# Kernel tuning notes

Hardware: AMD Instinct MI355X
Metric: run time of the kernel (lower is better)

## Reference

```python
import jax, jax.numpy as jnp
import numpy as np
from jax import lax

DEPTH_SIZE = 16


def _conv2d(x, w, b):
    # x: [B,C,H,W], w: [O,I,5,5], 'SAME' == padding=2 for k=5
    y = lax.conv_general_dilated(x, w, (1, 1), 'SAME',
                                 dimension_numbers=('NCHW', 'OIHW', 'NCHW'))
    return y + b[None, :, None, None]


def _bn(x, g, b, m, v):
    # eval-mode BatchNorm2d, eps=1e-5
    scale = g / jnp.sqrt(v + 1e-5)
    return (x - m[None, :, None, None]) * scale[None, :, None, None] + b[None, :, None, None]


def setup_inputs() -> dict:
    key = jax.random.key(0)
    ks = jax.random.split(key, 24)
    f32 = jnp.float32
    B, H, W = 1, 384, 384

    def cw(k, shape):
        fan_in = float(np.prod(shape[1:]))
        return jax.random.normal(k, shape, f32) / np.float32(np.sqrt(fan_in))

    inp = {
        'light':     jax.random.uniform(ks[0], (B, 3, H, W), f32),
        'albedo':    jax.random.uniform(ks[1], (B, 3, H, W), f32),
        'normals':   jax.random.normal(ks[2], (B, 3, H, W), f32),
        'positions': jax.random.normal(ks[3], (B, 3, H, W), f32),
        'c1_w': cw(ks[4], (32, 9, 5, 5)),  'c1_b': jnp.zeros((32,), f32),
        'bn1_g': jax.random.uniform(ks[5], (32,), f32, 0.5, 1.5),
        'bn1_b': jax.random.normal(ks[6], (32,), f32) * 0.1,
        'bn1_m': jax.random.normal(ks[7], (32,), f32) * 0.1,
        'bn1_v': jax.random.uniform(ks[8], (32,), f32, 0.5, 1.5),
        'c2_w': cw(ks[9], (8, 32, 5, 5)),  'c2_b': jnp.zeros((8,), f32),
        'bn2_g': jax.random.uniform(ks[10], (8,), f32, 0.5, 1.5),
        'bn2_b': jax.random.normal(ks[11], (8,), f32) * 0.1,
        'bn2_m': jax.random.normal(ks[12], (8,), f32) * 0.1,
        'bn2_v': jax.random.uniform(ks[13], (8,), f32, 0.5, 1.5),
        'c3_w': cw(ks[14], (1, 8, 5, 5)),  'c3_b': jnp.zeros((1,), f32),
        'bn3_g': jax.random.uniform(ks[15], (1,), f32, 0.5, 1.5),
        'bn3_b': jax.random.normal(ks[16], (1,), f32) * 0.1,
        'bn3_m': jax.random.normal(ks[17], (1,), f32) * 0.1,
        'bn3_v': jax.random.uniform(ks[18], (1,), f32, 0.5, 1.5),
        'f_w': cw(ks[19], (4, 4, 7, 7, 7)),
        # weight-channel bias = 1 keeps the divide-by-weight well conditioned
        'f_b': jnp.concatenate([jnp.zeros((3,), f32), jnp.ones((1,), f32)]),
    }
    return inp


def reference(light, albedo, normals, positions,
              c1_w, c1_b, bn1_g, bn1_b, bn1_m, bn1_v,
              c2_w, c2_b, bn2_g, bn2_b, bn2_m, bn2_v,
              c3_w, c3_b, bn3_g, bn3_b, bn3_m, bn3_v,
              f_w, f_b):
    D = DEPTH_SIZE
    B, _, H, W = light.shape

    # estimate_depth CNN on cat(light, albedo, normals) -> sigmoid embedding in (0,1)
    x = jnp.concatenate([light, albedo, normals], axis=1)           # [B,9,H,W]
    h = jax.nn.relu(_bn(_conv2d(x, c1_w, c1_b), bn1_g, bn1_b, bn1_m, bn1_v))
    h = jax.nn.relu(_bn(_conv2d(h, c2_w, c2_b), bn2_g, bn2_b, bn2_m, bn2_v))
    emb = jax.nn.sigmoid(_bn(_conv2d(h, c3_w, c3_b), bn3_g, bn3_b, bn3_m, bn3_v))  # [B,1,H,W]

    # quantize depth into bin index (long() == floor for positive values)
    depth = jnp.floor(emb[:, 0] * (D - 1e-5)).astype(jnp.int32)     # [B,H,W], in [0,15]

    # project: scatter per-pixel (light, 1) into the 16-slot depth volume
    wl = jnp.concatenate([light, jnp.ones((B, 1, H, W), light.dtype)], axis=1)   # [B,4,H,W]
    onehot = (depth[:, None, :, :] == jnp.arange(D)[None, :, None, None]).astype(light.dtype)  # [B,D,H,W]
    vol = wl[:, :, None, :, :] * onehot[:, None, :, :, :]           # [B,4,D,H,W]

    # dense 7^3 Conv3d filter, padding=3 == 'SAME'
    fvol = lax.conv_general_dilated(vol, f_w, (1, 1, 1), 'SAME',
                                    dimension_numbers=('NCDHW', 'OIDHW', 'NCDHW'))
    fvol = fvol + f_b[None, :, None, None, None]                    # [B,4,D,H,W]

    # unproject: gather back at each pixel's depth bin
    idx = jnp.broadcast_to(depth[:, None, None, :, :], (B, 4, 1, H, W))
    gathered = jnp.take_along_axis(fvol, idx, axis=2)[:, :, 0]      # [B,4,H,W]

    filtered_light, weight = gathered[:, :3], gathered[:, 3:4]
    return (filtered_light / weight) * albedo                       # [B,3,H,W]
```

## Files before the change

kernel.cpp:

```cpp
#include <hip/hip_runtime.h>
#include <math.h>

#define HW 384
#define PLANE (HW*HW)

#define WT1_OFF   0
#define SC1_OFF   7296
#define SH1_OFF   7328
#define WT2_OFF   7360
#define SC2_OFF   13760
#define SH2_OFF   13768
#define W3_OFF    13776
#define SC3_OFF   13976
#define SH3_OFF   13977
#define FWT_OFF   13984
#define H1_OFF    32768
#define H2_OFF    (32768 + 32*PLANE)

__global__ void prep_kernel(
    const float* __restrict__ c1w, const float* __restrict__ c1b,
    const float* __restrict__ g1, const float* __restrict__ b1,
    const float* __restrict__ m1, const float* __restrict__ v1,
    const float* __restrict__ c2w, const float* __restrict__ c2b,
    const float* __restrict__ g2, const float* __restrict__ b2,
    const float* __restrict__ m2, const float* __restrict__ v2,
    const float* __restrict__ c3w, const float* __restrict__ c3b,
    const float* __restrict__ g3, const float* __restrict__ b3,
    const float* __restrict__ m3, const float* __restrict__ v3,
    const float* __restrict__ fw, float* __restrict__ W)
{
    int gid = blockIdx.x * 256 + threadIdx.x;
    int gstr = gridDim.x * 256;
    for (int i = gid; i < 7200; i += gstr) {
        int wu = i / 900, r = i % 900;
        int ct = r >> 2, o = r & 3;
        int oc = wu * 4 + o;
        W[WT1_OFF + i] = c1w[oc * 225 + ct];
    }
    for (int i = gid; i < 6400; i += gstr) {
        int gw = i / 400, r = i % 400;
        int cc2 = r / 200, r2 = r % 200, tap = r2 >> 3, o = r2 & 7;
        int cab = (gw >> 2) * 8 + (gw & 3) * 2 + cc2;
        W[WT2_OFF + i] = c2w[o * 800 + cab * 25 + tap];
    }
    for (int i = gid; i < 6860; i += gstr) {
        int s = i / 20, k = i % 20;
        float v = 0.f;
        if (k < 16) { int o = k >> 2, c = k & 3; v = fw[o * 1372 + c * 343 + s]; }
        W[FWT_OFF + i] = v;
    }
    if (blockIdx.x == 0) {
        int tid = threadIdx.x;
        if (tid < 32) {
            float sc = g1[tid] / sqrtf(v1[tid] + 1e-5f);
            W[SC1_OFF + tid] = sc;
            W[SH1_OFF + tid] = (c1b[tid] - m1[tid]) * sc + b1[tid];
        }
        if (tid < 8) {
            float sc = g2[tid] / sqrtf(v2[tid] + 1e-5f);
            W[SC2_OFF + tid] = sc;
            W[SH2_OFF + tid] = (c2b[tid] - m2[tid]) * sc + b2[tid];
        }
        if (tid < 200) W[W3_OFF + tid] = c3w[tid];
        if (tid == 0) {
            float sc = g3[0] / sqrtf(v3[0] + 1e-5f);
            W[SC3_OFF] = sc;
            W[SH3_OFF] = (c3b[0] - m3[0]) * sc + b3[0];
        }
    }
}

__global__ __launch_bounds__(512, 4) void conv1_kernel(
    const float* __restrict__ light, const float* __restrict__ albedo,
    const float* __restrict__ normals, const float* __restrict__ W,
    float* __restrict__ h1)
{
    __shared__ __align__(16) float tile[9 * 432];
    int tid = threadIdx.x;
    int wu = __builtin_amdgcn_readfirstlane(tid >> 6);
    int slot = tid & 63;
    int qx = slot & 7, ty = slot >> 3;
    int bx = blockIdx.x % 12, by = blockIdx.x / 12;
    int x0 = bx * 32, y0 = by * 8;

    if (tid < 432) {
        int p = tid;
        int py = p / 36, px = p % 36;
        int gy = y0 + py - 2, gx = x0 + px - 2;
        bool ok = ((unsigned)gy < (unsigned)HW) && ((unsigned)gx < (unsigned)HW);
        int gofs = ok ? (gy * HW + gx) : 0;
#pragma unroll
        for (int c = 0; c < 3; ++c) {
            float a = light[c * PLANE + gofs];
            float b = albedo[c * PLANE + gofs];
            float n = normals[c * PLANE + gofs];
            tile[(c    ) * 432 + p] = ok ? a : 0.f;
            tile[(c + 3) * 432 + p] = ok ? b : 0.f;
            tile[(c + 6) * 432 + p] = ok ? n : 0.f;
        }
    }
    __syncthreads();

    float acc[4][4];
#pragma unroll
    for (int o = 0; o < 4; ++o)
#pragma unroll
        for (int j = 0; j < 4; ++j) acc[o][j] = 0.f;

    const float* wbase = W + WT1_OFF + wu * 900;
#pragma unroll 1
    for (int c = 0; c < 9; ++c) {
        const float* bc = tile + c * 432;
        const float* wc = wbase + c * 100;
#pragma unroll
        for (int ky = 0; ky < 5; ++ky) {
            const float* rp = bc + (ty + ky) * 36 + qx * 4;
            float4 ra = *(const float4*)rp;
            float4 rb = *(const float4*)(rp + 4);
            float row[8] = {ra.x, ra.y, ra.z, ra.w, rb.x, rb.y, rb.z, rb.w};
#pragma unroll
            for (int kx = 0; kx < 5; ++kx) {
                float4 wA = *(const float4*)(wc + (ky * 5 + kx) * 4);
#pragma unroll
                for (int j = 0; j < 4; ++j) {
                    float v = row[kx + j];
                    acc[0][j] = fmaf(v, wA.x, acc[0][j]);
                    acc[1][j] = fmaf(v, wA.y, acc[1][j]);
                    acc[2][j] = fmaf(v, wA.z, acc[2][j]);
                    acc[3][j] = fmaf(v, wA.w, acc[3][j]);
                }
            }
        }
    }

    int pix = (y0 + ty) * HW + x0 + qx * 4;
#pragma unroll
    for (int o = 0; o < 4; ++o) {
        int oc = wu * 4 + o;
        float sc = W[SC1_OFF + oc], sh = W[SH1_OFF + oc];
        float4 rv;
        rv.x = fmaxf(fmaf(acc[o][0], sc, sh), 0.f);
        rv.y = fmaxf(fmaf(acc[o][1], sc, sh), 0.f);
        rv.z = fmaxf(fmaf(acc[o][2], sc, sh), 0.f);
        rv.w = fmaxf(fmaf(acc[o][3], sc, sh), 0.f);
        *(float4*)&h1[oc * PLANE + pix] = rv;
    }
}

__global__ __launch_bounds__(256, 4) void conv2_kernel(
    const float* __restrict__ h1, const float* __restrict__ W,
    float* __restrict__ h2p)
{
    __shared__ __align__(16) float lds[4608];
    int tid = threadIdx.x;
    int wu = __builtin_amdgcn_readfirstlane(tid >> 6);
    int slot = tid & 63;
    int qx = slot & 7, ty = slot >> 3;
    int bid = blockIdx.x;
    int q = bid & 3, sp = bid >> 2;
    int bx = sp % 12, by = sp / 12;
    int x0 = bx * 32, y0 = by * 8;
    int cbase = q * 8;

    for (int p = tid; p < 432; p += 256) {
        int py = p / 36, px = p % 36;
        int gy = y0 + py - 2, gx = x0 + px - 2;
        bool ok = ((unsigned)gy < (unsigned)HW) && ((unsigned)gx < (unsigned)HW);
        int gofs = ok ? (gy * HW + gx) : 0;
#pragma unroll
        for (int cc = 0; cc < 8; ++cc) {
            float v = h1[(cbase + cc) * PLANE + gofs];
            lds[cc * 432 + p] = ok ? v : 0.f;
        }
    }
    __syncthreads();

    float acc[8][4];
#pragma unroll
    for (int o = 0; o < 8; ++o)
#pragma unroll
        for (int j = 0; j < 4; ++j) acc[o][j] = 0.f;

    int gw = q * 4 + wu;
#pragma unroll 1
    for (int cc2 = 0; cc2 < 2; ++cc2) {
        const float* bc = lds + (2 * wu + cc2) * 432;
        const float* wc = W + WT2_OFF + gw * 400 + cc2 * 200;
#pragma unroll
        for (int ky = 0; ky < 5; ++ky) {
            const float* rp = bc + (ty + ky) * 36 + qx * 4;
            float4 ra = *(const float4*)rp;
            float4 rb = *(const float4*)(rp + 4);
            float row[8] = {ra.x, ra.y, ra.z, ra.w, rb.x, rb.y, rb.z, rb.w};
#pragma unroll
            for (int kx = 0; kx < 5; ++kx) {
                const float* wt = wc + (ky * 5 + kx) * 8;
                float4 wA = *(const float4*)wt;
                float4 wB = *(const float4*)(wt + 4);
#pragma unroll
                for (int j = 0; j < 4; ++j) {
                    float v = row[kx + j];
                    acc[0][j] = fmaf(v, wA.x, acc[0][j]);
                    acc[1][j] = fmaf(v, wA.y, acc[1][j]);
                    acc[2][j] = fmaf(v, wA.z, acc[2][j]);
                    acc[3][j] = fmaf(v, wA.w, acc[3][j]);
                    acc[4][j] = fmaf(v, wB.x, acc[4][j]);
                    acc[5][j] = fmaf(v, wB.y, acc[5][j]);
                    acc[6][j] = fmaf(v, wB.z, acc[6][j]);
                    acc[7][j] = fmaf(v, wB.w, acc[7][j]);
                }
            }
        }
    }
    __syncthreads();

    if (wu >= 2) {
        float* pp = lds + (wu - 2) * 2304 + slot * 36;
#pragma unroll
        for (int o = 0; o < 8; ++o)
            *(float4*)(pp + o * 4) = make_float4(acc[o][0], acc[o][1], acc[o][2], acc[o][3]);
    }
    __syncthreads();
    if (wu < 2) {
        const float* pp = lds + wu * 2304 + slot * 36;
#pragma unroll
        for (int o = 0; o < 8; ++o) {
            float4 t = *(const float4*)(pp + o * 4);
            acc[o][0] += t.x; acc[o][1] += t.y; acc[o][2] += t.z; acc[o][3] += t.w;
        }
    }
    __syncthreads();
    if (wu == 1) {
        float* pp = lds + slot * 36;
#pragma unroll
        for (int o = 0; o < 8; ++o)
            *(float4*)(pp + o * 4) = make_float4(acc[o][0], acc[o][1], acc[o][2], acc[o][3]);
    }
    __syncthreads();
    if (wu == 0) {
        const float* pp = lds + slot * 36;
        int pix = (y0 + ty) * HW + x0 + qx * 4;
#pragma unroll
        for (int o = 0; o < 8; ++o) {
            float4 t = *(const float4*)(pp + o * 4);
            float4 rv;
            rv.x = acc[o][0] + t.x; rv.y = acc[o][1] + t.y;
            rv.z = acc[o][2] + t.z; rv.w = acc[o][3] + t.w;
            *(float4*)&h2p[(q * 8 + o) * PLANE + pix] = rv;
        }
    }
}

__global__ __launch_bounds__(256, 4) void final_kernel(
    const float* __restrict__ light, const float* __restrict__ albedo,
    const float* __restrict__ h2p, const float* __restrict__ W,
    const float* __restrict__ fb, float* __restrict__ out)
{
    __shared__ __align__(16) float u[6860];
    __shared__ float ltile[3][14][38];
    __shared__ int   dtile[14][38];

    int tid = threadIdx.x;
    int tx = tid & 31, ty = tid >> 5;
    int bx = blockIdx.x % 12, by = blockIdx.x / 12;
    int x0 = bx * 32 - 3, y0 = by * 8 - 3;
    int x2 = x0 - 2, y2 = y0 - 2;

    for (int p = tid; p < 756; p += 256) {
        int r = p / 42, cpx = p % 42;
        int gy = y2 + r, gx = x2 + cpx;
        bool ok = ((unsigned)gy < (unsigned)HW) && ((unsigned)gx < (unsigned)HW);
        int gofs = ok ? (gy * HW + gx) : 0;
#pragma unroll
        for (int c = 0; c < 8; ++c) {
            float t = ((h2p[c * PLANE + gofs] + h2p[(c + 8) * PLANE + gofs])
                     + h2p[(c + 16) * PLANE + gofs]) + h2p[(c + 24) * PLANE + gofs];
            float rr = fmaxf(fmaf(t, W[SC2_OFF + c], W[SH2_OFF + c]), 0.f);
            u[c * 756 + p] = ok ? rr : 0.f;
        }
    }
    for (int p = tid; p < 532; p += 256) {
        int py = p / 38, px = p % 38;
        int gy = y0 + py, gx = x0 + px;
        bool ok = ((unsigned)gy < (unsigned)HW) && ((unsigned)gx < (unsigned)HW);
        int gofs = ok ? (gy * HW + gx) : 0;
#pragma unroll
        for (int c = 0; c < 3; ++c) {
            float lv = light[c * PLANE + gofs];
            ltile[c][py][px] = ok ? lv : 0.f;
        }
    }
    __syncthreads();

    for (int p = tid; p < 532; p += 256) {
        int py = p / 38, px = p % 38;
        int gy = y0 + py, gx = x0 + px;
        bool ok = ((unsigned)gy < (unsigned)HW) && ((unsigned)gx < (unsigned)HW);
        int d = -1000;
        if (ok) {
            float a = 0.f;
#pragma unroll 1
            for (int c = 0; c < 8; ++c) {
#pragma unroll
                for (int ky = 0; ky < 5; ++ky) {
#pragma unroll
                    for (int kx = 0; kx < 5; ++kx) {
                        a = fmaf(u[c * 756 + (py + ky) * 42 + (px + kx)],
                                 W[W3_OFF + (c * 5 + ky) * 5 + kx], a);
                    }
                }
            }
            float y = fmaf(a, W[SC3_OFF], W[SH3_OFF]);
            float s = 1.f / (1.f + expf(-y));
            d = (int)floorf(s * (16.f - 1e-5f));
        }
        dtile[py][px] = d;
    }
    __syncthreads();

    for (int i = tid; i < 6860; i += 256) u[i] = W[FWT_OFF + i];
    __syncthreads();

    int d0 = dtile[ty + 3][tx + 3];
    float a0 = fb[0], a1 = fb[1], a2 = fb[2], a3 = fb[3];

#pragma unroll 1
    for (int dy = 0; dy < 7; ++dy) {
#pragma unroll
        for (int dx = 0; dx < 7; ++dx) {
            int dd = dtile[ty + dy][tx + dx];
            int dz = dd - d0 + 3;
            if ((unsigned)dz < 7u) {
                int s = (dz * 7 + dy) * 7 + dx;
                const float* fs = u + s * 20;
                float4 w0 = *(const float4*)(fs);
                float4 w1 = *(const float4*)(fs + 4);
                float4 w2 = *(const float4*)(fs + 8);
                float4 w3 = *(const float4*)(fs + 12);
                float l0 = ltile[0][ty + dy][tx + dx];
                float l1 = ltile[1][ty + dy][tx + dx];
                float l2 = ltile[2][ty + dy][tx + dx];
                a0 += l0 * w0.x + l1 * w0.y + l2 * w0.z + w0.w;
                a1 += l0 * w1.x + l1 * w1.y + l2 * w1.z + w1.w;
                a2 += l0 * w2.x + l1 * w2.y + l2 * w2.z + w2.w;
                a3 += l0 * w3.x + l1 * w3.y + l2 * w3.z + w3.w;
            }
        }
    }

    int gy = by * 8 + ty, gx = bx * 32 + tx;
    int pix = gy * HW + gx;
    out[0 * PLANE + pix] = a0 / a3 * albedo[0 * PLANE + pix];
    out[1 * PLANE + pix] = a1 / a3 * albedo[1 * PLANE + pix];
    out[2 * PLANE + pix] = a2 / a3 * albedo[2 * PLANE + pix];
}

extern "C" void kernel_launch(void* const* d_in, const int* in_sizes, int n_in,
                              void* d_out, int out_size, void* d_ws, size_t ws_size,
                              hipStream_t stream) {
    const float* light     = (const float*)d_in[0];
    const float* albedo    = (const float*)d_in[1];
    const float* normals   = (const float*)d_in[2];
    const float* c1_w = (const float*)d_in[4];
    const float* c1_b = (const float*)d_in[5];
    const float* bn1_g = (const float*)d_in[6];
    const float* bn1_b = (const float*)d_in[7];
    const float* bn1_m = (const float*)d_in[8];
    const float* bn1_v = (const float*)d_in[9];
    const float* c2_w = (const float*)d_in[10];
    const float* c2_b = (const float*)d_in[11];
    const float* bn2_g = (const float*)d_in[12];
    const float* bn2_b = (const float*)d_in[13];
    const float* bn2_m = (const float*)d_in[14];
    const float* bn2_v = (const float*)d_in[15];
    const float* c3_w = (const float*)d_in[16];
    const float* c3_b = (const float*)d_in[17];
    const float* bn3_g = (const float*)d_in[18];
    const float* bn3_b = (const float*)d_in[19];
    const float* bn3_m = (const float*)d_in[20];
    const float* bn3_v = (const float*)d_in[21];
    const float* f_w = (const float*)d_in[22];
    const float* f_b = (const float*)d_in[23];

    float* W = (float*)d_ws;
    float* h1 = W + H1_OFF;
    float* h2p = W + H2_OFF;
    float* out = (float*)d_out;

    hipLaunchKernelGGL(prep_kernel, dim3(16), dim3(256), 0, stream,
                       c1_w, c1_b, bn1_g, bn1_b, bn1_m, bn1_v,
                       c2_w, c2_b, bn2_g, bn2_b, bn2_m, bn2_v,
                       c3_w, c3_b, bn3_g, bn3_b, bn3_m, bn3_v,
                       f_w, W);
    hipLaunchKernelGGL(conv1_kernel, dim3(576), dim3(512), 0, stream,
                       light, albedo, normals, W, h1);
    hipLaunchKernelGGL(conv2_kernel, dim3(2304), dim3(256), 0, stream,
                       h1, W, h2p);
    hipLaunchKernelGGL(final_kernel, dim3(576), dim3(256), 0, stream,
                       light, albedo, h2p, W, f_b, out);
}
```

Baseline: 104.6 us.

## Rebalance conv1/conv2 split: halve conv1 blocks, full-channel conv2 with in-block reduction

```diff
diff --git a/kernel.cpp b/kernel.cpp
--- a/kernel.cpp
+++ b/kernel.cpp
@@ -32,15 +32,13 @@
     int gid = blockIdx.x * 256 + threadIdx.x;
     int gstr = gridDim.x * 256;
     for (int i = gid; i < 7200; i += gstr) {
-        int wu = i / 900, r = i % 900;
+        int gw = i / 900, r = i % 900;
         int ct = r >> 2, o = r & 3;
-        int oc = wu * 4 + o;
+        int oc = gw * 4 + o;
         W[WT1_OFF + i] = c1w[oc * 225 + ct];
     }
     for (int i = gid; i < 6400; i += gstr) {
-        int gw = i / 400, r = i % 400;
-        int cc2 = r / 200, r2 = r % 200, tap = r2 >> 3, o = r2 & 7;
-        int cab = (gw >> 2) * 8 + (gw & 3) * 2 + cc2;
+        int cab = i / 200, r2 = i % 200, tap = r2 >> 3, o = r2 & 7;
         W[WT2_OFF + i] = c2w[o * 800 + cab * 25 + tap];
     }
     for (int i = gid; i < 6860; i += gstr) {
@@ -70,7 +68,7 @@
     }
 }
 
-__global__ __launch_bounds__(512, 4) void conv1_kernel(
+__global__ __launch_bounds__(256, 4) void conv1_kernel(
     const float* __restrict__ light, const float* __restrict__ albedo,
     const float* __restrict__ normals, const float* __restrict__ W,
     float* __restrict__ h1)
@@ -80,11 +78,12 @@
     int wu = __builtin_amdgcn_readfirstlane(tid >> 6);
     int slot = tid & 63;
     int qx = slot & 7, ty = slot >> 3;
-    int bx = blockIdx.x % 12, by = blockIdx.x / 12;
+    int bid = blockIdx.x;
+    int half = bid & 1, sp = bid >> 1;
+    int bx = sp % 12, by = sp / 12;
     int x0 = bx * 32, y0 = by * 8;
 
-    if (tid < 432) {
-        int p = tid;
+    for (int p = tid; p < 432; p += 256) {
         int py = p / 36, px = p % 36;
         int gy = y0 + py - 2, gx = x0 + px - 2;
         bool ok = ((unsigned)gy < (unsigned)HW) && ((unsigned)gx < (unsigned)HW);
@@ -107,7 +106,8 @@
 #pragma unroll
         for (int j = 0; j < 4; ++j) acc[o][j] = 0.f;
 
-    const float* wbase = W + WT1_OFF + wu * 900;
+    int gw = half * 4 + wu;
+    const float* wbase = W + WT1_OFF + gw * 900;
 #pragma unroll 1
     for (int c = 0; c < 9; ++c) {
         const float* bc = tile + c * 432;
@@ -136,7 +136,7 @@
     int pix = (y0 + ty) * HW + x0 + qx * 4;
 #pragma unroll
     for (int o = 0; o < 4; ++o) {
-        int oc = wu * 4 + o;
+        int oc = gw * 4 + o;
         float sc = W[SC1_OFF + oc], sh = W[SH1_OFF + oc];
         float4 rv;
         rv.x = fmaxf(fmaf(acc[o][0], sc, sh), 0.f);
@@ -147,30 +147,28 @@
     }
 }
 
-__global__ __launch_bounds__(256, 4) void conv2_kernel(
+__global__ __launch_bounds__(512, 4) void conv2_kernel(
     const float* __restrict__ h1, const float* __restrict__ W,
-    float* __restrict__ h2p)
+    float* __restrict__ h2)
 {
-    __shared__ __align__(16) float lds[4608];
+    __shared__ __align__(16) float lds[13824];
     int tid = threadIdx.x;
     int wu = __builtin_amdgcn_readfirstlane(tid >> 6);
     int slot = tid & 63;
     int qx = slot & 7, ty = slot >> 3;
-    int bid = blockIdx.x;
-    int q = bid & 3, sp = bid >> 2;
-    int bx = sp % 12, by = sp / 12;
+    int bx = blockIdx.x % 12, by = blockIdx.x / 12;
     int x0 = bx * 32, y0 = by * 8;
-    int cbase = q * 8;
-
-    for (int p = tid; p < 432; p += 256) {
+
+    if (tid < 432) {
+        int p = tid;
         int py = p / 36, px = p % 36;
         int gy = y0 + py - 2, gx = x0 + px - 2;
         bool ok = ((unsigned)gy < (unsigned)HW) && ((unsigned)gx < (unsigned)HW);
         int gofs = ok ? (gy * HW + gx) : 0;
-#pragma unroll
-        for (int cc = 0; cc < 8; ++cc) {
-            float v = h1[(cbase + cc) * PLANE + gofs];
-            lds[cc * 432 + p] = ok ? v : 0.f;
+#pragma unroll 4
+        for (int c = 0; c < 32; ++c) {
+            float v = h1[c * PLANE + gofs];
+            lds[c * 432 + p] = ok ? v : 0.f;
         }
     }
     __syncthreads();
@@ -181,11 +179,11 @@
 #pragma unroll
         for (int j = 0; j < 4; ++j) acc[o][j] = 0.f;
 
-    int gw = q * 4 + wu;
 #pragma unroll 1
-    for (int cc2 = 0; cc2 < 2; ++cc2) {
-        const float* bc = lds + (2 * wu + cc2) * 432;
-        const float* wc = W + WT2_OFF + gw * 400 + cc2 * 200;
+    for (int cc2 = 0; cc2 < 4; ++cc2) {
+        int cab = wu * 4 + cc2;
+        const float* bc = lds + cab * 432;
+        const float* wc = W + WT2_OFF + cab * 200;
 #pragma unroll
         for (int ky = 0; ky < 5; ++ky) {
             const float* rp = bc + (ty + ky) * 36 + qx * 4;
@@ -214,14 +212,14 @@
     }
     __syncthreads();
 
-    if (wu >= 2) {
-        float* pp = lds + (wu - 2) * 2304 + slot * 36;
+    if (wu >= 4) {
+        float* pp = lds + (wu - 4) * 2304 + slot * 36;
 #pragma unroll
         for (int o = 0; o < 8; ++o)
             *(float4*)(pp + o * 4) = make_float4(acc[o][0], acc[o][1], acc[o][2], acc[o][3]);
     }
     __syncthreads();
-    if (wu < 2) {
+    if (wu < 4) {
         const float* pp = lds + wu * 2304 + slot * 36;
 #pragma unroll
         for (int o = 0; o < 8; ++o) {
@@ -230,6 +228,22 @@
         }
     }
     __syncthreads();
+    if (wu == 2 || wu == 3) {
+        float* pp = lds + (wu - 2) * 2304 + slot * 36;
+#pragma unroll
+        for (int o = 0; o < 8; ++o)
+            *(float4*)(pp + o * 4) = make_float4(acc[o][0], acc[o][1], acc[o][2], acc[o][3]);
+    }
+    __syncthreads();
+    if (wu < 2) {
+        const float* pp = lds + wu * 2304 + slot * 36;
+#pragma unroll
+        for (int o = 0; o < 8; ++o) {
+            float4 t = *(const float4*)(pp + o * 4);
+            acc[o][0] += t.x; acc[o][1] += t.y; acc[o][2] += t.z; acc[o][3] += t.w;
+        }
+    }
+    __syncthreads();
     if (wu == 1) {
         float* pp = lds + slot * 36;
 #pragma unroll
@@ -243,17 +257,22 @@
 #pragma unroll
         for (int o = 0; o < 8; ++o) {
             float4 t = *(const float4*)(pp + o * 4);
+            float s0 = acc[o][0] + t.x, s1 = acc[o][1] + t.y;
+            float s2 = acc[o][2] + t.z, s3 = acc[o][3] + t.w;
+            float sc = W[SC2_OFF + o], sh = W[SH2_OFF + o];
             float4 rv;
-            rv.x = acc[o][0] + t.x; rv.y = acc[o][1] + t.y;
-            rv.z = acc[o][2] + t.z; rv.w = acc[o][3] + t.w;
-            *(float4*)&h2p[(q * 8 + o) * PLANE + pix] = rv;
+            rv.x = fmaxf(fmaf(s0, sc, sh), 0.f);
+            rv.y = fmaxf(fmaf(s1, sc, sh), 0.f);
+            rv.z = fmaxf(fmaf(s2, sc, sh), 0.f);
+            rv.w = fmaxf(fmaf(s3, sc, sh), 0.f);
+            *(float4*)&h2[o * PLANE + pix] = rv;
         }
     }
 }
 
 __global__ __launch_bounds__(256, 4) void final_kernel(
     const float* __restrict__ light, const float* __restrict__ albedo,
-    const float* __restrict__ h2p, const float* __restrict__ W,
+    const float* __restrict__ h2, const float* __restrict__ W,
     const float* __restrict__ fb, float* __restrict__ out)
 {
     __shared__ __align__(16) float u[6860];
@@ -273,10 +292,8 @@
         int gofs = ok ? (gy * HW + gx) : 0;
 #pragma unroll
         for (int c = 0; c < 8; ++c) {
-            float t = ((h2p[c * PLANE + gofs] + h2p[(c + 8) * PLANE + gofs])
-                     + h2p[(c + 16) * PLANE + gofs]) + h2p[(c + 24) * PLANE + gofs];
-            float rr = fmaxf(fmaf(t, W[SC2_OFF + c], W[SH2_OFF + c]), 0.f);
-            u[c * 756 + p] = ok ? rr : 0.f;
+            float v = h2[c * PLANE + gofs];
+            u[c * 756 + p] = ok ? v : 0.f;
         }
     }
     for (int p = tid; p < 532; p += 256) {
@@ -384,7 +401,7 @@
 
     float* W = (float*)d_ws;
     float* h1 = W + H1_OFF;
-    float* h2p = W + H2_OFF;
+    float* h2 = W + H2_OFF;
     float* out = (float*)d_out;
 
     hipLaunchKernelGGL(prep_kernel, dim3(16), dim3(256), 0, stream,
@@ -392,10 +409,10 @@
                        c2_w, c2_b, bn2_g, bn2_b, bn2_m, bn2_v,
                        c3_w, c3_b, bn3_g, bn3_b, bn3_m, bn3_v,
                        f_w, W);
-    hipLaunchKernelGGL(conv1_kernel, dim3(576), dim3(512), 0, stream,
+    hipLaunchKernelGGL(conv1_kernel, dim3(1152), dim3(256), 0, stream,
                        light, albedo, normals, W, h1);
-    hipLaunchKernelGGL(conv2_kernel, dim3(2304), dim3(256), 0, stream,
-                       h1, W, h2p);
+    hipLaunchKernelGGL(conv2_kernel, dim3(576), dim3(512), 0, stream,
+                       h1, W, h2);
     hipLaunchKernelGGL(final_kernel, dim3(576), dim3(256), 0, stream,
-                       light, albedo, h2p, W, f_b, out);
+                       light, albedo, h2, W, f_b, out);
 }
```

New measurement: 101.5 us. -2.9%, faster.

## Split conv1 blocks by output-channel halves and precompute conv2 partial-sum reduction

Applied to the files above, without the earlier changes.

```diff
diff --git a/kernel.cpp b/kernel.cpp
--- a/kernel.cpp
+++ b/kernel.cpp
@@ -15,7 +15,8 @@
 #define SH3_OFF   13977
 #define FWT_OFF   13984
 #define H1_OFF    32768
-#define H2_OFF    (32768 + 32*PLANE)
+#define H2P_OFF   (32768 + 32*PLANE)
+#define H2S_OFF   (32768 + 64*PLANE)
 
 __global__ void prep_kernel(
     const float* __restrict__ c1w, const float* __restrict__ c1b,
@@ -32,9 +33,9 @@
     int gid = blockIdx.x * 256 + threadIdx.x;
     int gstr = gridDim.x * 256;
     for (int i = gid; i < 7200; i += gstr) {
-        int wu = i / 900, r = i % 900;
+        int gw = i / 900, r = i % 900;
         int ct = r >> 2, o = r & 3;
-        int oc = wu * 4 + o;
+        int oc = gw * 4 + o;
         W[WT1_OFF + i] = c1w[oc * 225 + ct];
     }
     for (int i = gid; i < 6400; i += gstr) {
@@ -70,7 +71,7 @@
     }
 }
 
-__global__ __launch_bounds__(512, 4) void conv1_kernel(
+__global__ __launch_bounds__(256, 4) void conv1_kernel(
     const float* __restrict__ light, const float* __restrict__ albedo,
     const float* __restrict__ normals, const float* __restrict__ W,
     float* __restrict__ h1)
@@ -80,11 +81,12 @@
     int wu = __builtin_amdgcn_readfirstlane(tid >> 6);
     int slot = tid & 63;
     int qx = slot & 7, ty = slot >> 3;
-    int bx = blockIdx.x % 12, by = blockIdx.x / 12;
+    int bid = blockIdx.x;
+    int half = bid & 1, sp = bid >> 1;
+    int bx = sp % 12, by = sp / 12;
     int x0 = bx * 32, y0 = by * 8;
 
-    if (tid < 432) {
-        int p = tid;
+    for (int p = tid; p < 432; p += 256) {
         int py = p / 36, px = p % 36;
         int gy = y0 + py - 2, gx = x0 + px - 2;
         bool ok = ((unsigned)gy < (unsigned)HW) && ((unsigned)gx < (unsigned)HW);
@@ -107,7 +109,8 @@
 #pragma unroll
         for (int j = 0; j < 4; ++j) acc[o][j] = 0.f;
 
-    const float* wbase = W + WT1_OFF + wu * 900;
+    int gw = half * 4 + wu;
+    const float* wbase = W + WT1_OFF + gw * 900;
 #pragma unroll 1
     for (int c = 0; c < 9; ++c) {
         const float* bc = tile + c * 432;
@@ -136,7 +139,7 @@
     int pix = (y0 + ty) * HW + x0 + qx * 4;
 #pragma unroll
     for (int o = 0; o < 4; ++o) {
-        int oc = wu * 4 + o;
+        int oc = gw * 4 + o;
         float sc = W[SC1_OFF + oc], sh = W[SH1_OFF + oc];
         float4 rv;
         rv.x = fmaxf(fmaf(acc[o][0], sc, sh), 0.f);
@@ -251,9 +254,34 @@
     }
 }
 
+__global__ __launch_bounds__(256) void combine_kernel(
+    const float* __restrict__ h2p, const float* __restrict__ W,
+    float* __restrict__ h2)
+{
+    int i = blockIdx.x * 256 + threadIdx.x;
+    int o = i / (PLANE / 4);
+    int p4 = i - o * (PLANE / 4);
+    int idx = o * PLANE + p4 * 4;
+    float4 t0 = *(const float4*)&h2p[idx];
+    float4 t1 = *(const float4*)&h2p[idx + 8 * PLANE];
+    float4 t2 = *(const float4*)&h2p[idx + 16 * PLANE];
+    float4 t3 = *(const float4*)&h2p[idx + 24 * PLANE];
+    float s0 = ((t0.x + t1.x) + t2.x) + t3.x;
+    float s1 = ((t0.y + t1.y) + t2.y) + t3.y;
+    float s2 = ((t0.z + t1.z) + t2.z) + t3.z;
+    float s3 = ((t0.w + t1.w) + t2.w) + t3.w;
+    float sc = W[SC2_OFF + o], sh = W[SH2_OFF + o];
+    float4 rv;
+    rv.x = fmaxf(fmaf(s0, sc, sh), 0.f);
+    rv.y = fmaxf(fmaf(s1, sc, sh), 0.f);
+    rv.z = fmaxf(fmaf(s2, sc, sh), 0.f);
+    rv.w = fmaxf(fmaf(s3, sc, sh), 0.f);
+    *(float4*)&h2[idx] = rv;
+}
+
 __global__ __launch_bounds__(256, 4) void final_kernel(
     const float* __restrict__ light, const float* __restrict__ albedo,
-    const float* __restrict__ h2p, const float* __restrict__ W,
+    const float* __restrict__ h2, const float* __restrict__ W,
     const float* __restrict__ fb, float* __restrict__ out)
 {
     __shared__ __align__(16) float u[6860];
@@ -273,10 +301,8 @@
         int gofs = ok ? (gy * HW + gx) : 0;
 #pragma unroll
         for (int c = 0; c < 8; ++c) {
-            float t = ((h2p[c * PLANE + gofs] + h2p[(c + 8) * PLANE + gofs])
-                     + h2p[(c + 16) * PLANE + gofs]) + h2p[(c + 24) * PLANE + gofs];
-            float rr = fmaxf(fmaf(t, W[SC2_OFF + c], W[SH2_OFF + c]), 0.f);
-            u[c * 756 + p] = ok ? rr : 0.f;
+            float v = h2[c * PLANE + gofs];
+            u[c * 756 + p] = ok ? v : 0.f;
         }
     }
     for (int p = tid; p < 532; p += 256) {
@@ -384,7 +410,8 @@
 
     float* W = (float*)d_ws;
     float* h1 = W + H1_OFF;
-    float* h2p = W + H2_OFF;
+    float* h2p = W + H2P_OFF;
+    float* h2 = W + H2S_OFF;
     float* out = (float*)d_out;
 
     hipLaunchKernelGGL(prep_kernel, dim3(16), dim3(256), 0, stream,
@@ -392,10 +419,12 @@
                        c2_w, c2_b, bn2_g, bn2_b, bn2_m, bn2_v,
                        c3_w, c3_b, bn3_g, bn3_b, bn3_m, bn3_v,
                        f_w, W);
-    hipLaunchKernelGGL(conv1_kernel, dim3(576), dim3(512), 0, stream,
+    hipLaunchKernelGGL(conv1_kernel, dim3(1152), dim3(256), 0, stream,
                        light, albedo, normals, W, h1);
     hipLaunchKernelGGL(conv2_kernel, dim3(2304), dim3(256), 0, stream,
                        h1, W, h2p);
+    hipLaunchKernelGGL(combine_kernel, dim3(1152), dim3(256), 0, stream,
+                       h2p, W, h2);
     hipLaunchKernelGGL(final_kernel, dim3(576), dim3(256), 0, stream,
-                       light, albedo, h2p, W, f_b, out);
-}
+                       light, albedo, h2, W, f_b, out);
+}
```

After: 95.59 us. 8.6% less time.
